# Kernel optimization log

Measured on AMD Instinct MI355X. Metric: run time of the kernel, lower is better.

The kernel has to match this reference:

```python
import jax, jax.numpy as jnp
import numpy as np

D_MODEL = 1024
N_HEADS = 16
D_HEAD = D_MODEL // N_HEADS
INIT_GATE = -5.0


def setup_inputs() -> dict:
    key = jax.random.key(0)
    ks = jax.random.split(key, 11)
    B, S, D = 2, 2048, D_MODEL
    lim = 1.0 / np.sqrt(D)  # torch Linear default init range
    def lin(kw, kb):
        W = jax.random.uniform(kw, (D, D), jnp.float32, -lim, lim)
        b = jax.random.uniform(kb, (D,), jnp.float32, -lim, lim)
        return W, b
    W_Q, b_Q = lin(ks[0], ks[1])
    W_K, b_K = lin(ks[2], ks[3])
    W_V, b_V = lin(ks[4], ks[5])
    W_O, b_O = lin(ks[6], ks[7])
    return {
        "low_freq": jax.random.normal(ks[8], (B, S, D), jnp.float32),
        "high_freq": jax.random.normal(ks[9], (B, S, D), jnp.float32),
        "W_Q": W_Q, "b_Q": b_Q,
        "W_K": W_K, "b_K": b_K,
        "W_V": W_V, "b_V": b_V,
        "W_O": W_O, "b_O": b_O,
        "gamma": jnp.asarray(INIT_GATE, jnp.float32),
    }


def reference(low_freq, high_freq, W_Q, b_Q, W_K, b_K, W_V, b_V, W_O, b_O, gamma):
    B, S, D = low_freq.shape
    H, Dh = N_HEADS, D_HEAD
    # torch Linear: y = x @ W.T + b
    Q = (low_freq @ W_Q.T + b_Q).reshape(B, S, H, Dh).transpose(0, 2, 1, 3)
    K = (low_freq @ W_K.T + b_K).reshape(B, S, H, Dh).transpose(0, 2, 1, 3)
    V = (high_freq @ W_V.T + b_V).reshape(B, S, H, Dh).transpose(0, 2, 1, 3)
    scores = jnp.einsum("bhqd,bhkd->bhqk", Q, K) / jnp.sqrt(jnp.asarray(Dh, low_freq.dtype))
    attn = jax.nn.softmax(scores, axis=-1)
    ctx = jnp.einsum("bhqk,bhkd->bhqd", attn, V)
    ctx = ctx.transpose(0, 2, 1, 3).reshape(B, S, D)
    Z = ctx @ W_O.T + b_O
    beta = jax.nn.sigmoid(gamma)
    return low_freq + beta * Z
```

## Files before the change

kernel.cpp:

```cpp
#include <hip/hip_runtime.h>
#include <stdint.h>

#define D_MODEL 1024
#define N_HEADS 16
#define BB      2
#define SS      2048
#define MTOT    (BB*SS)
#define NXs     ((size_t)MTOT * D_MODEL)
#define NWs     ((size_t)D_MODEL * D_MODEL)

typedef __attribute__((ext_vector_type(8))) short bf16x8;
typedef __attribute__((ext_vector_type(4))) float f32x4;
typedef __attribute__((ext_vector_type(16))) float f32x16;

__device__ __forceinline__ ushort f2bf(float f) {
    union { float f; uint32_t u; } v; v.f = f;
    uint32_t u = v.u;
    return (ushort)((u + 0x7FFFu + ((u >> 16) & 1u)) >> 16);
}
__device__ __forceinline__ uint32_t pk2bf(float lo, float hi) {
    uint32_t r;
    asm("v_cvt_pk_bf16_f32 %0, %1, %2" : "=v"(r) : "v"(lo), "v"(hi));
    return r;
}
__device__ __forceinline__ float exp2_raw(float x) {
    float r;
    asm("v_exp_f32 %0, %1" : "=v"(r) : "v"(x));
    return r;
}
#define GLL16(gp, lp) __builtin_amdgcn_global_load_lds( \
    (const __attribute__((address_space(1))) void*)(gp), \
    (__attribute__((address_space(3))) void*)(lp), 16, 0, 0)

__global__ __launch_bounds__(256) void cvt_all(
    const float* __restrict__ s0, const float* __restrict__ s1,
    const float* __restrict__ s2, const float* __restrict__ s3,
    const float* __restrict__ s4, const float* __restrict__ s5,
    ushort* __restrict__ dst)
{
    size_t i = ((size_t)blockIdx.x * 256 + threadIdx.x) * 4;
    const float* src; size_t off;
    if (i < NXs)            { src = s0; off = i; }
    else if (i < 2 * NXs)   { src = s1; off = i - NXs; }
    else {
        size_t j = i - 2 * NXs;
        int sel = (int)(j >> 20);
        src = sel == 0 ? s2 : sel == 1 ? s3 : sel == 2 ? s4 : s5;
        off = j & (NWs - 1);
    }
    float4 v = *reinterpret_cast<const float4*>(src + off);
    ushort4 o;
    o.x = f2bf(v.x); o.y = f2bf(v.y); o.z = f2bf(v.z); o.w = f2bf(v.w);
    *reinterpret_cast<ushort4*>(dst + i) = o;
}

__global__ __launch_bounds__(512, 2) void qkv256(
    const ushort* __restrict__ Xl, const ushort* __restrict__ Xh,
    const ushort* __restrict__ Wqk, const ushort* __restrict__ Wv,
    const float* __restrict__ bq, const float* __restrict__ bk,
    const float* __restrict__ bv,
    ushort* __restrict__ QK, ushort* __restrict__ VT)
{
    extern __shared__ char dsm[];
    const int t = threadIdx.x, lane = t & 63, w = t >> 6;
    const int wr = w >> 2, wc = w & 3;
    const int c16 = lane & 15, kg = lane >> 4;
    const int xorv = (c16 & 7) << 4;

    const int bid = blockIdx.x;
    const ushort *Ain, *Win;
    int bm, bn, isV;
    if (bid < 128) {
        const int xcd = bid & 7, k = bid >> 3;
        Ain = Xl; Win = Wqk; isV = 0;
        bm = ((xcd >> 1) << 2) | (k >> 2);
        bn = ((xcd & 1) << 2) | (k & 3);
    } else {
        const int vid = bid - 128;
        const int xcd = vid & 7, k = vid >> 3;
        Ain = Xh; Win = Wv; isV = 1;
        bm = (xcd << 1) | (k >> 2);
        bn = k & 3;
    }

    const int swcol = ((t & 7) * 8) ^ (((t >> 3) & 7) << 3);
    const ushort* Asrc = Ain + (size_t)(bm * 256 + (t >> 3)) * 1024 + swcol;
    const ushort* Bsrc = Win + (size_t)(bn * 256 + (t >> 3)) * 1024 + swcol;
    char* const ldsA = dsm;
    char* const ldsB = dsm + 65536;

#define STAGE_A(Tn, h, sl) do { \
    const ushort* _s = Asrc + (size_t)(h) * 128 * 1024 + (size_t)(Tn) * 64; \
    char* _d = ldsA + (sl) * 32768 + (h) * 16384 + t * 16; \
    GLL16(_s, _d); GLL16(_s + 64 * 1024, _d + 8192); } while (0)
#define STAGE_B(Tn, h, sl) do { \
    const ushort* _s = Bsrc + (size_t)(h) * 128 * 1024 + (size_t)(Tn) * 64; \
    char* _d = ldsB + (sl) * 32768 + (h) * 16384 + t * 16; \
    GLL16(_s, _d); GLL16(_s + 64 * 1024, _d + 8192); } while (0)

    f32x4 acc[8][4] = {};

    STAGE_A(0, 0, 0); STAGE_B(0, 0, 0);
    STAGE_A(0, 1, 0); STAGE_B(0, 1, 0);
    asm volatile("s_waitcnt vmcnt(0)" ::: "memory");
    __syncthreads();

    const char* Ahb = ldsA + wr * 16384;
    const char* Bhb = ldsB + (wc >> 1) * 16384;
    const int nbase = (wc & 1) * 64;

#pragma unroll 1
    for (int T = 0; T < 16; ++T) {
        const int slot = T & 1;
        const char* Ab = Ahb + slot * 32768;
        const char* Bb = Bhb + slot * 32768;
        bf16x8 af[2][4], bfr[2][4];

        if (T + 1 < 16) {
            STAGE_A(T + 1, 0, slot ^ 1);
            STAGE_B(T + 1, 0, slot ^ 1);
            STAGE_A(T + 1, 1, slot ^ 1);
            STAGE_B(T + 1, 1, slot ^ 1);
            asm volatile("s_waitcnt vmcnt(8)" ::: "memory");
        } else {
            asm volatile("s_waitcnt vmcnt(0)" ::: "memory");
        }
#pragma unroll
        for (int kk = 0; kk < 2; ++kk) {
#pragma unroll
            for (int mf = 0; mf < 4; ++mf)
                af[kk][mf] = *(const bf16x8*)(Ab +
                    (((mf * 16 + c16) * 128 + kk * 64 + kg * 16) ^ xorv));
#pragma unroll
            for (int nf = 0; nf < 4; ++nf)
                bfr[kk][nf] = *(const bf16x8*)(Bb +
                    (((nbase + nf * 16 + c16) * 128 + kk * 64 + kg * 16) ^ xorv));
        }
        __builtin_amdgcn_s_barrier();
        asm volatile("s_waitcnt lgkmcnt(0)" ::: "memory");
        __builtin_amdgcn_sched_barrier(0);
        __builtin_amdgcn_s_setprio(1);
#pragma unroll
        for (int kk = 0; kk < 2; ++kk)
#pragma unroll
            for (int mf = 0; mf < 4; ++mf)
#pragma unroll
                for (int nf = 0; nf < 4; ++nf)
                    acc[mf][nf] = __builtin_amdgcn_mfma_f32_16x16x32_bf16(
                        af[kk][mf], bfr[kk][nf], acc[mf][nf], 0, 0, 0);
        __builtin_amdgcn_s_setprio(0);
        __builtin_amdgcn_s_barrier();

#pragma unroll
        for (int kk = 0; kk < 2; ++kk)
#pragma unroll
            for (int mf = 0; mf < 4; ++mf)
                af[kk][mf] = *(const bf16x8*)(Ab +
                    (((64 + mf * 16 + c16) * 128 + kk * 64 + kg * 16) ^ xorv));
        __builtin_amdgcn_s_barrier();
        asm volatile("s_waitcnt lgkmcnt(0)" ::: "memory");
        __builtin_amdgcn_sched_barrier(0);
        __builtin_amdgcn_s_setprio(1);
#pragma unroll
        for (int kk = 0; kk < 2; ++kk)
#pragma unroll
            for (int mf = 0; mf < 4; ++mf)
#pragma unroll
                for (int nf = 0; nf < 4; ++nf)
                    acc[4 + mf][nf] = __builtin_amdgcn_mfma_f32_16x16x32_bf16(
                        af[kk][mf], bfr[kk][nf], acc[4 + mf][nf], 0, 0, 0);
        __builtin_amdgcn_s_setprio(0);
        __builtin_amdgcn_s_barrier();
    }

    const int row0 = bm * 256 + wr * 128;
    const int col0w = wc * 64;
    if (!isV) {
#pragma unroll
        for (int nf = 0; nf < 4; ++nf) {
            const int col = bn * 256 + col0w + nf * 16 + c16;
            const float bv_ = (col < 1024 ? bq : bk)[col & 1023];
            const float sc  = (col < 1024 ? 0.125f * 1.44269504f : 1.f);
#pragma unroll
            for (int mf = 0; mf < 8; ++mf)
#pragma unroll
                for (int r = 0; r < 4; ++r) {
                    const int row = row0 + mf * 16 + kg * 4 + r;
                    QK[(size_t)row * 2048 + col] = f2bf((acc[mf][nf][r] + bv_) * sc);
                }
        }
    } else {
#pragma unroll
        for (int nf = 0; nf < 4; ++nf) {
            const int col = bn * 256 + col0w + nf * 16 + c16;
            const int h = col >> 6, d = col & 63;
            const float bv_ = bv[col];
#pragma unroll
            for (int mf = 0; mf < 8; ++mf) {
                const int rw0 = row0 + mf * 16 + kg * 4;
                const int b_ = rw0 >> 11, s0 = rw0 & 2047;
                ushort4 ov;
                ov.x = f2bf(acc[mf][nf][0] + bv_);
                ov.y = f2bf(acc[mf][nf][1] + bv_);
                ov.z = f2bf(acc[mf][nf][2] + bv_);
                ov.w = f2bf(acc[mf][nf][3] + bv_);
                *reinterpret_cast<ushort4*>(VT + ((size_t)(b_ * 16 + h) * 64 + d) * 2048 + s0) = ov;
            }
        }
    }
#undef STAGE_A
#undef STAGE_B
}

__global__ __launch_bounds__(256) void o_gemm(
    const ushort* __restrict__ Cb, const ushort* __restrict__ Wo,
    const float* __restrict__ bo, const float* __restrict__ low,
    const float* __restrict__ gamma, float* __restrict__ outf)
{
    __shared__ __align__(16) ushort As[2][128 * 32];
    __shared__ __align__(16) ushort Bs[2][64 * 32];
    const int t = threadIdx.x, lane = t & 63, w = t >> 6;
    const int wr = w >> 1, wc = w & 1, c16 = lane & 15, kg = lane >> 4;
    const int bid = blockIdx.x;
    const int xcd = bid & 7, i = bid >> 3;
    const int bm = xcd * 4 + (i >> 4), bn = i & 15;

    const int sr = t >> 2, scb = (t & 3) * 8;
    const ushort* Ag = Cb + (size_t)(bm * 128 + sr) * 1024 + scb;
    const ushort* Wg = Wo + (size_t)(bn * 64 + sr) * 1024 + scb;

    f32x4 acc[4][2] = {};

    GLL16(Ag,             (char*)As[0] + t * 16);
    GLL16(Ag + 64 * 1024, (char*)As[0] + t * 16 + 4096);
    GLL16(Wg,             (char*)Bs[0] + t * 16);
    __syncthreads();
    Ag += 32; Wg += 32;

    int cur = 0;
    for (int kt = 0; kt < 32; ++kt) {
        if (kt < 31) {
            char* ad = (char*)As[cur ^ 1] + t * 16;
            char* bd = (char*)Bs[cur ^ 1] + t * 16;
            GLL16(Ag,             ad);
            GLL16(Ag + 64 * 1024, ad + 4096);
            GLL16(Wg,             bd);
            Ag += 32; Wg += 32;
        }
        bf16x8 af[4], bfr[2];
#pragma unroll
        for (int m = 0; m < 4; ++m)
            af[m] = *(const bf16x8*)((const char*)As[cur] + (wr * 64 + m * 16 + c16) * 64 + kg * 16);
#pragma unroll
        for (int n = 0; n < 2; ++n)
            bfr[n] = *(const bf16x8*)((const char*)Bs[cur] + (wc * 32 + n * 16 + c16) * 64 + kg * 16);
#pragma unroll
        for (int m = 0; m < 4; ++m)
#pragma unroll
            for (int n = 0; n < 2; ++n)
                acc[m][n] = __builtin_amdgcn_mfma_f32_16x16x32_bf16(af[m], bfr[n], acc[m][n], 0, 0, 0);
        __syncthreads();
        cur ^= 1;
    }

    const float beta = 1.f / (1.f + __expf(-gamma[0]));
#pragma unroll
    for (int n = 0; n < 2; ++n) {
        const int col = bn * 64 + wc * 32 + n * 16 + c16;
        const float bv_ = bo[col];
#pragma unroll
        for (int m = 0; m < 4; ++m)
#pragma unroll
            for (int r = 0; r < 4; ++r) {
                const int row = bm * 128 + wr * 64 + m * 16 + kg * 4 + r;
                const size_t off = (size_t)row * 1024 + col;
                outf[off] = low[off] + beta * (acc[m][n][r] + bv_);
            }
    }
}

__global__ __launch_bounds__(512, 4) void flash_attn7(
    const ushort* __restrict__ QK, const ushort* __restrict__ VT,
    ushort* __restrict__ CTX)
{
    __shared__ __align__(16) char smem[65536];
    const int t = threadIdx.x;
    const int lane = t & 63, w = t >> 6;
    const int l31 = lane & 31, hi = lane >> 5;
    const int g = w >> 2, wg = w & 3;

    const int bid = blockIdx.x;
    const int j   = bid >> 3;
    const int hbi = (bid & 7) * 4 + (j >> 4);
    const int qb  = j & 15;
    const int b   = hbi >> 4, h = hbi & 15;

    const size_t qrow = (size_t)b * SS + qb * 128 + wg * 32 + l31;
    const ushort* Qp = QK + qrow * 2048 + h * 64;
    bf16x8 qf[4];
#pragma unroll
    for (int ks = 0; ks < 4; ++ks)
        qf[ks] = *reinterpret_cast<const bf16x8*>(Qp + ks * 16 + hi * 8);

    const int t256 = t & 255;
    const int r0 = t256 >> 3;
    const int cb = ((t256 & 7) ^ (r0 & 7)) << 4;
    const ushort* Ksrc = QK + ((size_t)b * SS + r0) * 2048 + 1024 + h * 64 + (cb >> 1);
    const ushort* Vsrc = VT + ((size_t)(b * N_HEADS + h) * 64 + r0) * SS + (cb >> 1);

    char* const Kreg = smem + g * 16384;
    char* const Vreg = smem + 32768 + g * 16384;

    constexpr short ONE = (short)0x3F80;
    const bf16x8 kones = {ONE, ONE, ONE, ONE, ONE, ONE, ONE, ONE};

    f32x16 o0 = {}, o1 = {}, sacc = {};

    {
        const ushort* Kn = Ksrc + (size_t)g * 64 * 2048;
        const ushort* Vn = Vsrc + g * 64;
        GLL16(Kn,             Kreg + t256 * 16);
        GLL16(Kn + 32 * 2048, Kreg + t256 * 16 + 4096);
        GLL16(Vn,             Vreg + t256 * 16);
        GLL16(Vn + 32 * SS,   Vreg + t256 * 16 + 4096);
    }
    __syncthreads();

    const ushort* Kpf = Ksrc + (size_t)(g + 2) * 64 * 2048;
    const ushort* Vpf = Vsrc + (g + 2) * 64;

    int cur = 0;
    for (int kt2 = 0; kt2 < 16; ++kt2) {
        if (kt2 < 15) {
            char* kd = Kreg + (cur ^ 1) * 8192 + t256 * 16;
            char* vd = Vreg + (cur ^ 1) * 8192 + t256 * 16;
            GLL16(Kpf,             kd);
            GLL16(Kpf + 32 * 2048, kd + 4096);
            GLL16(Vpf,             vd);
            GLL16(Vpf + 32 * SS,   vd + 4096);
            Kpf += (size_t)2 * 64 * 2048;
            Vpf += 2 * 64;
        }
        const char* Kb_ = Kreg + cur * 8192;
        const char* Vb_ = Vreg + cur * 8192;

        f32x16 sa0 = {}, sa1 = {};
        __builtin_amdgcn_s_setprio(1);
#pragma unroll
        for (int ks = 0; ks < 4; ++ks) {
            const int x0 = l31 * 128 + ((ks * 32 + hi * 16) ^ ((l31 & 7) << 4));
            bf16x8 k0 = *reinterpret_cast<const bf16x8*>(Kb_ + x0);
            bf16x8 k1 = *reinterpret_cast<const bf16x8*>(Kb_ + x0 + 32 * 128);
            sa0 = __builtin_amdgcn_mfma_f32_32x32x16_bf16(k0, qf[ks], sa0, 0, 0, 0);
            sa1 = __builtin_amdgcn_mfma_f32_32x32x16_bf16(k1, qf[ks], sa1, 0, 0, 0);
        }
        __builtin_amdgcn_s_setprio(0);

        float p[32];
#pragma unroll
        for (int i = 0; i < 16; ++i) { p[i] = exp2_raw(sa0[i]); p[16 + i] = exp2_raw(sa1[i]); }

        __builtin_amdgcn_s_setprio(1);
#pragma unroll
        for (int kc = 0; kc < 4; ++kc) {
            const int bq_ = (kc >> 1) * 16 + (kc & 1) * 8;
            uint32_t A0 = pk2bf(p[bq_ + 0], p[bq_ + 1]);
            uint32_t A1 = pk2bf(p[bq_ + 2], p[bq_ + 3]);
            uint32_t B0 = pk2bf(p[bq_ + 4], p[bq_ + 5]);
            uint32_t B1 = pk2bf(p[bq_ + 6], p[bq_ + 7]);
            asm("v_permlane32_swap_b32 %0, %1" : "+v"(A0), "+v"(B0));
            asm("v_permlane32_swap_b32 %0, %1" : "+v"(A1), "+v"(B1));
            union { uint32_t u[4]; bf16x8 v; } pa;
            pa.u[0] = A0; pa.u[1] = A1; pa.u[2] = B0; pa.u[3] = B1;
            const int xv = l31 * 128 + ((kc * 32 + hi * 16) ^ ((l31 & 7) << 4));
            bf16x8 v0 = *reinterpret_cast<const bf16x8*>(Vb_ + xv);
            bf16x8 v1 = *reinterpret_cast<const bf16x8*>(Vb_ + xv + 32 * 128);
            o0 = __builtin_amdgcn_mfma_f32_32x32x16_bf16(v0, pa.v, o0, 0, 0, 0);
            o1 = __builtin_amdgcn_mfma_f32_32x32x16_bf16(v1, pa.v, o1, 0, 0, 0);
            sacc = __builtin_amdgcn_mfma_f32_32x32x16_bf16(kones, pa.v, sacc, 0, 0, 0);
        }
        __builtin_amdgcn_s_setprio(0);
        __syncthreads();
        cur ^= 1;
    }

    const float lrun = sacc[0];

    float* O1 = (float*)smem;
    float* L1 = (float*)(smem + 128 * 66 * 4);
    const int ql = wg * 32 + l31;
    if (g == 1) {
#pragma unroll
        for (int r = 0; r < 16; ++r) {
            const int d = (r & 3) + 8 * (r >> 2) + 4 * hi;
            O1[ql * 66 + d]      = o0[r];
            O1[ql * 66 + 32 + d] = o1[r];
        }
        if (hi == 0) L1[ql] = lrun;
    }
    __syncthreads();
    if (g == 0) {
        const float invl = 1.f / (lrun + L1[ql]);
        ushort* Cp = CTX + qrow * D_MODEL + h * 64;
#pragma unroll
        for (int dt = 0; dt < 2; ++dt) {
            const f32x16 o = dt ? o1 : o0;
#pragma unroll
            for (int gg = 0; gg < 4; ++gg) {
                ushort4 ov;
#pragma unroll
                for (int jj = 0; jj < 4; ++jj) {
                    const int r = gg * 4 + jj;
                    const int d = dt * 32 + gg * 8 + hi * 4 + jj;
                    const float v = (o[r] + O1[ql * 66 + d]) * invl;
                    ((ushort*)&ov)[jj] = f2bf(v);
                }
                *reinterpret_cast<ushort4*>(Cp + dt * 32 + gg * 8 + hi * 4) = ov;
            }
        }
    }
}

extern "C" void kernel_launch(void* const* d_in, const int* in_sizes, int n_in,
                              void* d_out, int out_size, void* d_ws, size_t ws_size,
                              hipStream_t stream) {
    const float* low   = (const float*)d_in[0];
    const float* high  = (const float*)d_in[1];
    const float* Wq    = (const float*)d_in[2];
    const float* bq    = (const float*)d_in[3];
    const float* Wk    = (const float*)d_in[4];
    const float* bk    = (const float*)d_in[5];
    const float* Wv    = (const float*)d_in[6];
    const float* bv    = (const float*)d_in[7];
    const float* Wo    = (const float*)d_in[8];
    const float* bo    = (const float*)d_in[9];
    const float* gamma = (const float*)d_in[10];
    float* out = (float*)d_out;

    ushort* ws  = (ushort*)d_ws;
    ushort* Xl  = ws;
    ushort* Xh  = Xl  + NXs;
    ushort* Wqb = Xh  + NXs;
    ushort* Wkb = Wqb + NWs;
    ushort* Wvb = Wkb + NWs;
    ushort* Wob = Wvb + NWs;
    ushort* QKb = Wob + NWs;
    ushort* VTb = QKb + 2 * NXs;
    ushort* Cb  = VTb + NXs;
    (void)Wkb;

    const int cvt_blocks = (int)((2 * NXs + 4 * NWs) / 4 / 256);
    cvt_all<<<cvt_blocks, 256, 0, stream>>>(low, high, Wq, Wk, Wv, Wo, ws);

    static int attr_set = 0;
    if (!attr_set) {
        hipFuncSetAttribute((const void*)qkv256,
                            hipFuncAttributeMaxDynamicSharedMemorySize, 131072);
        attr_set = 1;
    }
    qkv256<<<192, 512, 131072, stream>>>(Xl, Xh, Wqb, Wvb, bq, bk, bv, QKb, VTb);

    flash_attn7<<<512, 512, 0, stream>>>(QKb, VTb, Cb);

    o_gemm<<<512, 256, 0, stream>>>(Cb, Wob, bo, low, gamma, out);
}
```

Measured before the change: 118.6 us.

## Fuse fp32-to-bf16 conversion of inputs and weights into QKV GEMM staging

Removes the separate conversion kernel for the activations and the Q/K/V weights. The QKV GEMM now loads fp32 tiles into registers, converts them to bf16 with packed converts and writes them to LDS, interleaved with the MFMA phases. Only W_O is still converted by a small standalone kernel. This avoids a full fp32 read plus bf16 write and re-read pass over the inputs, but replaces asynchronous direct-to-LDS loads with register-staged loads that double the global bytes per tile and add vmcnt(0) waits inside the main loop.

```diff
diff --git a/kernel.cpp b/kernel.cpp
--- a/kernel.cpp
+++ b/kernel.cpp
@@ -32,31 +32,18 @@
     (const __attribute__((address_space(1))) void*)(gp), \
     (__attribute__((address_space(3))) void*)(lp), 16, 0, 0)
 
-__global__ __launch_bounds__(256) void cvt_all(
-    const float* __restrict__ s0, const float* __restrict__ s1,
-    const float* __restrict__ s2, const float* __restrict__ s3,
-    const float* __restrict__ s4, const float* __restrict__ s5,
-    ushort* __restrict__ dst)
-{
+__global__ __launch_bounds__(256) void cvt_wo(const float* __restrict__ in, ushort* __restrict__ out) {
     size_t i = ((size_t)blockIdx.x * 256 + threadIdx.x) * 4;
-    const float* src; size_t off;
-    if (i < NXs)            { src = s0; off = i; }
-    else if (i < 2 * NXs)   { src = s1; off = i - NXs; }
-    else {
-        size_t j = i - 2 * NXs;
-        int sel = (int)(j >> 20);
-        src = sel == 0 ? s2 : sel == 1 ? s3 : sel == 2 ? s4 : s5;
-        off = j & (NWs - 1);
-    }
-    float4 v = *reinterpret_cast<const float4*>(src + off);
+    float4 v = *reinterpret_cast<const float4*>(in + i);
     ushort4 o;
     o.x = f2bf(v.x); o.y = f2bf(v.y); o.z = f2bf(v.z); o.w = f2bf(v.w);
-    *reinterpret_cast<ushort4*>(dst + i) = o;
+    *reinterpret_cast<ushort4*>(out + i) = o;
 }
 
 __global__ __launch_bounds__(512, 2) void qkv256(
-    const ushort* __restrict__ Xl, const ushort* __restrict__ Xh,
-    const ushort* __restrict__ Wqk, const ushort* __restrict__ Wv,
+    const float* __restrict__ Xl, const float* __restrict__ Xh,
+    const float* __restrict__ Wq, const float* __restrict__ Wk,
+    const float* __restrict__ Wv,
     const float* __restrict__ bq, const float* __restrict__ bk,
     const float* __restrict__ bv,
     ushort* __restrict__ QK, ushort* __restrict__ VT)
@@ -68,41 +55,68 @@
     const int xorv = (c16 & 7) << 4;
 
     const int bid = blockIdx.x;
-    const ushort *Ain, *Win;
-    int bm, bn, isV;
+    const float *Ainf, *Winf;
+    int bm, bn, isV, wrow0;
     if (bid < 128) {
         const int xcd = bid & 7, k = bid >> 3;
-        Ain = Xl; Win = Wqk; isV = 0;
+        Ainf = Xl; isV = 0;
         bm = ((xcd >> 1) << 2) | (k >> 2);
         bn = ((xcd & 1) << 2) | (k & 3);
+        if (bn < 4) { Winf = Wq; wrow0 = bn * 256; }
+        else        { Winf = Wk; wrow0 = (bn - 4) * 256; }
     } else {
         const int vid = bid - 128;
         const int xcd = vid & 7, k = vid >> 3;
-        Ain = Xh; Win = Wv; isV = 1;
+        Ainf = Xh; isV = 1;
         bm = (xcd << 1) | (k >> 2);
         bn = k & 3;
-    }
-
-    const int swcol = ((t & 7) * 8) ^ (((t >> 3) & 7) << 3);
-    const ushort* Asrc = Ain + (size_t)(bm * 256 + (t >> 3)) * 1024 + swcol;
-    const ushort* Bsrc = Win + (size_t)(bn * 256 + (t >> 3)) * 1024 + swcol;
+        Winf = Wv; wrow0 = bn * 256;
+    }
+
+    const int srow = t >> 3;
+    const int swcol = ((t & 7) * 8) ^ ((srow & 7) << 3);
+    const float* Af = Ainf + (size_t)(bm * 256 + srow) * 1024 + swcol;
+    const float* Bf = Winf + (size_t)(wrow0 + srow) * 1024 + swcol;
     char* const ldsA = dsm;
     char* const ldsB = dsm + 65536;
-
-#define STAGE_A(Tn, h, sl) do { \
-    const ushort* _s = Asrc + (size_t)(h) * 128 * 1024 + (size_t)(Tn) * 64; \
-    char* _d = ldsA + (sl) * 32768 + (h) * 16384 + t * 16; \
-    GLL16(_s, _d); GLL16(_s + 64 * 1024, _d + 8192); } while (0)
-#define STAGE_B(Tn, h, sl) do { \
-    const ushort* _s = Bsrc + (size_t)(h) * 128 * 1024 + (size_t)(Tn) * 64; \
-    char* _d = ldsB + (sl) * 32768 + (h) * 16384 + t * 16; \
-    GLL16(_s, _d); GLL16(_s + 64 * 1024, _d + 8192); } while (0)
+    char* const ldsAw = ldsA + t * 16;
+    char* const ldsBw = ldsB + t * 16;
 
     f32x4 acc[8][4] = {};
-
-    STAGE_A(0, 0, 0); STAGE_B(0, 0, 0);
-    STAGE_A(0, 1, 0); STAGE_B(0, 1, 0);
-    asm volatile("s_waitcnt vmcnt(0)" ::: "memory");
+    float4 lr[4][2];
+
+    {
+#pragma unroll
+        for (int ri = 0; ri < 4; ++ri) {
+            lr[ri][0] = *(const float4*)(Af + ri * 64 * 1024);
+            lr[ri][1] = *(const float4*)(Af + ri * 64 * 1024 + 4);
+        }
+        asm volatile("s_waitcnt vmcnt(0)" ::: "memory");
+#pragma unroll
+        for (int ri = 0; ri < 4; ++ri) {
+            union { uint32_t u[4]; bf16x8 v; } pk;
+            pk.u[0] = pk2bf(lr[ri][0].x, lr[ri][0].y);
+            pk.u[1] = pk2bf(lr[ri][0].z, lr[ri][0].w);
+            pk.u[2] = pk2bf(lr[ri][1].x, lr[ri][1].y);
+            pk.u[3] = pk2bf(lr[ri][1].z, lr[ri][1].w);
+            *(bf16x8*)(ldsAw + (ri >> 1) * 16384 + (ri & 1) * 8192) = pk.v;
+        }
+#pragma unroll
+        for (int ri = 0; ri < 4; ++ri) {
+            lr[ri][0] = *(const float4*)(Bf + ri * 64 * 1024);
+            lr[ri][1] = *(const float4*)(Bf + ri * 64 * 1024 + 4);
+        }
+        asm volatile("s_waitcnt vmcnt(0)" ::: "memory");
+#pragma unroll
+        for (int ri = 0; ri < 4; ++ri) {
+            union { uint32_t u[4]; bf16x8 v; } pk;
+            pk.u[0] = pk2bf(lr[ri][0].x, lr[ri][0].y);
+            pk.u[1] = pk2bf(lr[ri][0].z, lr[ri][0].w);
+            pk.u[2] = pk2bf(lr[ri][1].x, lr[ri][1].y);
+            pk.u[3] = pk2bf(lr[ri][1].z, lr[ri][1].w);
+            *(bf16x8*)(ldsBw + (ri >> 1) * 16384 + (ri & 1) * 8192) = pk.v;
+        }
+    }
     __syncthreads();
 
     const char* Ahb = ldsA + wr * 16384;
@@ -114,16 +128,15 @@
         const int slot = T & 1;
         const char* Ab = Ahb + slot * 32768;
         const char* Bb = Bhb + slot * 32768;
+        const int cb2 = (T + 1) * 64;
         bf16x8 af[2][4], bfr[2][4];
 
         if (T + 1 < 16) {
-            STAGE_A(T + 1, 0, slot ^ 1);
-            STAGE_B(T + 1, 0, slot ^ 1);
-            STAGE_A(T + 1, 1, slot ^ 1);
-            STAGE_B(T + 1, 1, slot ^ 1);
-            asm volatile("s_waitcnt vmcnt(8)" ::: "memory");
-        } else {
-            asm volatile("s_waitcnt vmcnt(0)" ::: "memory");
+#pragma unroll
+            for (int ri = 0; ri < 4; ++ri) {
+                lr[ri][0] = *(const float4*)(Af + ri * 64 * 1024 + cb2);
+                lr[ri][1] = *(const float4*)(Af + ri * 64 * 1024 + cb2 + 4);
+            }
         }
 #pragma unroll
         for (int kk = 0; kk < 2; ++kk) {
@@ -151,6 +164,24 @@
         __builtin_amdgcn_s_setprio(0);
         __builtin_amdgcn_s_barrier();
 
+        if (T + 1 < 16) {
+            asm volatile("s_waitcnt vmcnt(0)" ::: "memory");
+            char* const dstA = ldsAw + (slot ^ 1) * 32768;
+#pragma unroll
+            for (int ri = 0; ri < 4; ++ri) {
+                union { uint32_t u[4]; bf16x8 v; } pk;
+                pk.u[0] = pk2bf(lr[ri][0].x, lr[ri][0].y);
+                pk.u[1] = pk2bf(lr[ri][0].z, lr[ri][0].w);
+                pk.u[2] = pk2bf(lr[ri][1].x, lr[ri][1].y);
+                pk.u[3] = pk2bf(lr[ri][1].z, lr[ri][1].w);
+                *(bf16x8*)(dstA + (ri >> 1) * 16384 + (ri & 1) * 8192) = pk.v;
+            }
+#pragma unroll
+            for (int ri = 0; ri < 4; ++ri) {
+                lr[ri][0] = *(const float4*)(Bf + ri * 64 * 1024 + cb2);
+                lr[ri][1] = *(const float4*)(Bf + ri * 64 * 1024 + cb2 + 4);
+            }
+        }
 #pragma unroll
         for (int kk = 0; kk < 2; ++kk)
 #pragma unroll
@@ -170,6 +201,20 @@
                     acc[4 + mf][nf] = __builtin_amdgcn_mfma_f32_16x16x32_bf16(
                         af[kk][mf], bfr[kk][nf], acc[4 + mf][nf], 0, 0, 0);
         __builtin_amdgcn_s_setprio(0);
+        if (T + 1 < 16) {
+            asm volatile("s_waitcnt vmcnt(0)" ::: "memory");
+            char* const dstB = ldsBw + (slot ^ 1) * 32768;
+#pragma unroll
+            for (int ri = 0; ri < 4; ++ri) {
+                union { uint32_t u[4]; bf16x8 v; } pk;
+                pk.u[0] = pk2bf(lr[ri][0].x, lr[ri][0].y);
+                pk.u[1] = pk2bf(lr[ri][0].z, lr[ri][0].w);
+                pk.u[2] = pk2bf(lr[ri][1].x, lr[ri][1].y);
+                pk.u[3] = pk2bf(lr[ri][1].z, lr[ri][1].w);
+                *(bf16x8*)(dstB + (ri >> 1) * 16384 + (ri & 1) * 8192) = pk.v;
+            }
+            asm volatile("s_waitcnt lgkmcnt(0)" ::: "memory");
+        }
         __builtin_amdgcn_s_barrier();
     }
 
@@ -208,8 +253,6 @@
             }
         }
     }
-#undef STAGE_A
-#undef STAGE_B
 }
 
 __global__ __launch_bounds__(256) void o_gemm(
@@ -438,19 +481,10 @@
     float* out = (float*)d_out;
 
     ushort* ws  = (ushort*)d_ws;
-    ushort* Xl  = ws;
-    ushort* Xh  = Xl  + NXs;
-    ushort* Wqb = Xh  + NXs;
-    ushort* Wkb = Wqb + NWs;
-    ushort* Wvb = Wkb + NWs;
-    ushort* Wob = Wvb + NWs;
+    ushort* Wob = ws;
     ushort* QKb = Wob + NWs;
     ushort* VTb = QKb + 2 * NXs;
     ushort* Cb  = VTb + NXs;
-    (void)Wkb;
-
-    const int cvt_blocks = (int)((2 * NXs + 4 * NWs) / 4 / 256);
-    cvt_all<<<cvt_blocks, 256, 0, stream>>>(low, high, Wq, Wk, Wv, Wo, ws);
 
     static int attr_set = 0;
     if (!attr_set) {
@@ -458,7 +492,9 @@
                             hipFuncAttributeMaxDynamicSharedMemorySize, 131072);
         attr_set = 1;
     }
-    qkv256<<<192, 512, 131072, stream>>>(Xl, Xh, Wqb, Wvb, bq, bk, bv, QKb, VTb);
+    qkv256<<<192, 512, 131072, stream>>>(low, high, Wq, Wk, Wv, bq, bk, bv, QKb, VTb);
+
+    cvt_wo<<<NWs / 1024, 256, 0, stream>>>(Wo, Wob);
 
     flash_attn7<<<512, 512, 0, stream>>>(QKb, VTb, Cb);
 
```

Result: slower. 127.8 us (+7.8%).

## Retile output GEMM to 64x64 swizzled tiles and replace ones-MFMA row sum

Applied to the files above, without the earlier changes.

The output projection GEMM moves from 128x64 tiles with K-step 32 to 64x64 tiles with K-step 64 and XOR-swizzled LDS, doubling the grid to 1024 blocks. The aim is more blocks for better CU occupancy and fewer bank conflicts, at the cost of lower reuse per tile. In flash attention, the softmax denominator is now summed in fp32 registers plus a cross-half permlane swap instead of an extra MFMA against a ones vector. That removes a third of the PV-stage MFMAs and also changes the rounding of the normaliser, since the sum no longer goes through bf16-rounded probabilities.

```diff
diff --git a/kernel.cpp b/kernel.cpp
--- a/kernel.cpp
+++ b/kernel.cpp
@@ -217,64 +217,75 @@
     const float* __restrict__ bo, const float* __restrict__ low,
     const float* __restrict__ gamma, float* __restrict__ outf)
 {
-    __shared__ __align__(16) ushort As[2][128 * 32];
-    __shared__ __align__(16) ushort Bs[2][64 * 32];
+    __shared__ __align__(16) ushort As[2][64 * 64];
+    __shared__ __align__(16) ushort Bs[2][64 * 64];
     const int t = threadIdx.x, lane = t & 63, w = t >> 6;
     const int wr = w >> 1, wc = w & 1, c16 = lane & 15, kg = lane >> 4;
+    const int xorv = (c16 & 7) << 4;
     const int bid = blockIdx.x;
     const int xcd = bid & 7, i = bid >> 3;
-    const int bm = xcd * 4 + (i >> 4), bn = i & 15;
-
-    const int sr = t >> 2, scb = (t & 3) * 8;
-    const ushort* Ag = Cb + (size_t)(bm * 128 + sr) * 1024 + scb;
-    const ushort* Wg = Wo + (size_t)(bn * 64 + sr) * 1024 + scb;
-
-    f32x4 acc[4][2] = {};
-
-    GLL16(Ag,             (char*)As[0] + t * 16);
-    GLL16(Ag + 64 * 1024, (char*)As[0] + t * 16 + 4096);
-    GLL16(Wg,             (char*)Bs[0] + t * 16);
+    const int bm = xcd * 8 + (i >> 4), bn = i & 15;
+
+    const int swc = ((t & 7) ^ ((t >> 3) & 7)) * 8;
+    const ushort* Ag = Cb + (size_t)(bm * 64 + (t >> 3)) * 1024 + swc;
+    const ushort* Wg = Wo + (size_t)(bn * 64 + (t >> 3)) * 1024 + swc;
+
+    f32x4 acc[2][2] = {};
+
+#define OSTAGE(Tn, sl) do { \
+    const int off_ = (Tn) * 64; \
+    char* a_ = (char*)As[sl] + t * 16; \
+    char* b_ = (char*)Bs[sl] + t * 16; \
+    GLL16(Ag + off_,             a_); \
+    GLL16(Ag + off_ + 32 * 1024, a_ + 4096); \
+    GLL16(Wg + off_,             b_); \
+    GLL16(Wg + off_ + 32 * 1024, b_ + 4096); } while (0)
+
+    OSTAGE(0, 0);
     __syncthreads();
-    Ag += 32; Wg += 32;
-
-    int cur = 0;
-    for (int kt = 0; kt < 32; ++kt) {
-        if (kt < 31) {
-            char* ad = (char*)As[cur ^ 1] + t * 16;
-            char* bd = (char*)Bs[cur ^ 1] + t * 16;
-            GLL16(Ag,             ad);
-            GLL16(Ag + 64 * 1024, ad + 4096);
-            GLL16(Wg,             bd);
-            Ag += 32; Wg += 32;
-        }
-        bf16x8 af[4], bfr[2];
-#pragma unroll
-        for (int m = 0; m < 4; ++m)
-            af[m] = *(const bf16x8*)((const char*)As[cur] + (wr * 64 + m * 16 + c16) * 64 + kg * 16);
-#pragma unroll
-        for (int n = 0; n < 2; ++n)
-            bfr[n] = *(const bf16x8*)((const char*)Bs[cur] + (wc * 32 + n * 16 + c16) * 64 + kg * 16);
-#pragma unroll
-        for (int m = 0; m < 4; ++m)
-#pragma unroll
-            for (int n = 0; n < 2; ++n)
-                acc[m][n] = __builtin_amdgcn_mfma_f32_16x16x32_bf16(af[m], bfr[n], acc[m][n], 0, 0, 0);
+
+#pragma unroll 1
+    for (int T = 0; T < 16; ++T) {
+        const int slot = T & 1;
+        if (T + 1 < 16) OSTAGE(T + 1, slot ^ 1);
+        const char* Ab = (const char*)As[slot];
+        const char* Bb = (const char*)Bs[slot];
+        bf16x8 af[2][2], bfr[2][2];
+#pragma unroll
+        for (int kk = 0; kk < 2; ++kk) {
+#pragma unroll
+            for (int mf = 0; mf < 2; ++mf)
+                af[kk][mf] = *(const bf16x8*)(Ab +
+                    (((wr * 32 + mf * 16 + c16) * 128 + kk * 64 + kg * 16) ^ xorv));
+#pragma unroll
+            for (int nf = 0; nf < 2; ++nf)
+                bfr[kk][nf] = *(const bf16x8*)(Bb +
+                    (((wc * 32 + nf * 16 + c16) * 128 + kk * 64 + kg * 16) ^ xorv));
+        }
+#pragma unroll
+        for (int kk = 0; kk < 2; ++kk)
+#pragma unroll
+            for (int mf = 0; mf < 2; ++mf)
+#pragma unroll
+                for (int nf = 0; nf < 2; ++nf)
+                    acc[mf][nf] = __builtin_amdgcn_mfma_f32_16x16x32_bf16(
+                        af[kk][mf], bfr[kk][nf], acc[mf][nf], 0, 0, 0);
         __syncthreads();
-        cur ^= 1;
-    }
+    }
+#undef OSTAGE
 
     const float beta = 1.f / (1.f + __expf(-gamma[0]));
 #pragma unroll
-    for (int n = 0; n < 2; ++n) {
-        const int col = bn * 64 + wc * 32 + n * 16 + c16;
+    for (int nf = 0; nf < 2; ++nf) {
+        const int col = bn * 64 + wc * 32 + nf * 16 + c16;
         const float bv_ = bo[col];
 #pragma unroll
-        for (int m = 0; m < 4; ++m)
+        for (int mf = 0; mf < 2; ++mf)
 #pragma unroll
             for (int r = 0; r < 4; ++r) {
-                const int row = bm * 128 + wr * 64 + m * 16 + kg * 4 + r;
+                const int row = bm * 64 + wr * 32 + mf * 16 + kg * 4 + r;
                 const size_t off = (size_t)row * 1024 + col;
-                outf[off] = low[off] + beta * (acc[m][n][r] + bv_);
+                outf[off] = low[off] + beta * (acc[mf][nf][r] + bv_);
             }
     }
 }
@@ -311,10 +322,8 @@
     char* const Kreg = smem + g * 16384;
     char* const Vreg = smem + 32768 + g * 16384;
 
-    constexpr short ONE = (short)0x3F80;
-    const bf16x8 kones = {ONE, ONE, ONE, ONE, ONE, ONE, ONE, ONE};
-
-    f32x16 o0 = {}, o1 = {}, sacc = {};
+    f32x16 o0 = {}, o1 = {};
+    float lsum = 0.f;
 
     {
         const ushort* Kn = Ksrc + (size_t)g * 64 * 2048;
@@ -359,6 +368,17 @@
         float p[32];
 #pragma unroll
         for (int i = 0; i < 16; ++i) { p[i] = exp2_raw(sa0[i]); p[16 + i] = exp2_raw(sa1[i]); }
+
+        {
+            float s16_[16];
+#pragma unroll
+            for (int i = 0; i < 16; ++i) s16_[i] = p[i] + p[i + 16];
+#pragma unroll
+            for (int st = 8; st >= 1; st >>= 1)
+#pragma unroll
+                for (int i = 0; i < st; ++i) s16_[i] += s16_[i + st];
+            lsum += s16_[0];
+        }
 
         __builtin_amdgcn_s_setprio(1);
 #pragma unroll
@@ -377,14 +397,15 @@
             bf16x8 v1 = *reinterpret_cast<const bf16x8*>(Vb_ + xv + 32 * 128);
             o0 = __builtin_amdgcn_mfma_f32_32x32x16_bf16(v0, pa.v, o0, 0, 0, 0);
             o1 = __builtin_amdgcn_mfma_f32_32x32x16_bf16(v1, pa.v, o1, 0, 0, 0);
-            sacc = __builtin_amdgcn_mfma_f32_32x32x16_bf16(kones, pa.v, sacc, 0, 0, 0);
         }
         __builtin_amdgcn_s_setprio(0);
         __syncthreads();
         cur ^= 1;
     }
 
-    const float lrun = sacc[0];
+    { float a_ = lsum, b_ = lsum;
+      asm("v_permlane32_swap_b32 %0, %1" : "+v"(a_), "+v"(b_));
+      lsum = a_ + b_; }
 
     float* O1 = (float*)smem;
     float* L1 = (float*)(smem + 128 * 66 * 4);
@@ -396,11 +417,11 @@
             O1[ql * 66 + d]      = o0[r];
             O1[ql * 66 + 32 + d] = o1[r];
         }
-        if (hi == 0) L1[ql] = lrun;
+        if (hi == 0) L1[ql] = lsum;
     }
     __syncthreads();
     if (g == 0) {
-        const float invl = 1.f / (lrun + L1[ql]);
+        const float invl = 1.f / (lsum + L1[ql]);
         ushort* Cp = CTX + qrow * D_MODEL + h * 64;
 #pragma unroll
         for (int dt = 0; dt < 2; ++dt) {
@@ -462,5 +483,5 @@
 
     flash_attn7<<<512, 512, 0, stream>>>(QKb, VTb, Cb);
 
-    o_gemm<<<512, 256, 0, stream>>>(Cb, Wob, bo, low, gamma, out);
-}
+    o_gemm<<<1024, 256, 0, stream>>>(Cb, Wob, bo, low, gamma, out);
+}
```

Result: faster. 108.7 us (-8.3%).
